# Optimization experiments

Hardware: AMD Instinct MI355X
Metric: run time of the kernel (lower is better)

## Reference

```python
import jax, jax.numpy as jnp
import numpy as np

DIST_THD = 2.0  # squared-distance threshold from my_chamfer_fn


def setup_inputs() -> dict:
    key = jax.random.key(0)
    k1, k2 = jax.random.split(key)
    pc1 = jax.random.normal(k1, (1, 16384, 3), dtype=jnp.float32)
    pc2 = jax.random.normal(k2, (1, 16384, 3), dtype=jnp.float32)
    return {"pc1": pc1, "pc2": pc2}


def _chamfer(x, y):
    # x: (N, P1, D), y: (N, P2, D). Squared pairwise distances (as pytorch3d knn_points).
    x2 = jnp.sum(x * x, axis=-1)                       # (N, P1)
    y2 = jnp.sum(y * y, axis=-1)                       # (N, P2)
    xy = jnp.einsum('npd,nqd->npq', x, y)              # (N, P1, P2)
    d2 = x2[:, :, None] + y2[:, None, :] - 2.0 * xy    # (N, P1, P2)
    cham_x = jnp.min(d2, axis=2)                       # (N, P1) NN dist x->y (K=1)
    cham_y = jnp.min(d2, axis=1)                       # (N, P2) NN dist y->x
    # threshold mask: distances >= 2 are zeroed
    cham_x = jnp.where(cham_x >= DIST_THD, 0.0, cham_x)
    cham_y = jnp.where(cham_y >= DIST_THD, 0.0, cham_y)
    N, P1, _ = x.shape
    P2 = y.shape[1]
    # point_reduction='mean' (lengths are full P), batch_reduction='mean'
    cx = jnp.sum(cham_x, axis=1) / P1
    cy = jnp.sum(cham_y, axis=1) / P2
    return jnp.sum(cx) / N + jnp.sum(cy) / N


def reference(pc1, pc2):
    # Chamfer loss between pc1 and pc2 (the kernel inside NSFP optimization);
    # normals are unused in this code path, so only the distance loss is returned.
    return _chamfer(pc1, pc2)
```

## Files before the change

kernel.cpp:

```cpp
#include <hip/hip_runtime.h>
#include <hip/hip_bf16.h>


constexpr int P      = 16384;
constexpr int BLK    = 256;
constexpr int NSEG   = 8;
constexpr int SEGPTS = P / NSEG;
constexpr int ROUND  = 1024;
constexpr int TILES  = ROUND / 32;
constexpr int ROWSB  = 256;

typedef short s8v  __attribute__((ext_vector_type(8)));
typedef float f16v __attribute__((ext_vector_type(16)));

static __device__ inline unsigned short bf16r(float f) {
    unsigned u = __float_as_uint(f);
    u = (u + 0x7FFFu + ((u >> 16) & 1u)) >> 16;
    return (unsigned short)u;
}
static __device__ inline float bf2f(unsigned short h) {
    return __uint_as_float(((unsigned)h) << 16);
}

static __device__ inline void encA(float a, float b, float c, unsigned e[8]) {
    const unsigned ONE = 0x3F80u;
    const float s = fmaf(a, a, fmaf(b, b, c * c));
    const unsigned short ah = bf16r(a), bh = bf16r(b), ch = bf16r(c);
    const unsigned short al = bf16r(a - bf2f(ah));
    const unsigned short bl = bf16r(b - bf2f(bh));
    const unsigned short cl = bf16r(c - bf2f(ch));
    const unsigned short sh = bf16r(s), sl = bf16r(s - bf2f(sh));
    e[0] = ah | ((unsigned)al << 16);
    e[1] = bh | ((unsigned)bl << 16);
    e[2] = ch | ((unsigned)cl << 16);
    e[3] = ah | ((unsigned)bh << 16);
    e[4] = ch | ((unsigned)sh << 16);
    e[5] = sl | (ONE << 16);
    e[6] = ONE;
    e[7] = 0;
}

static __device__ inline void encB(float a, float b, float c, unsigned e[8]) {
    const unsigned ONE = 0x3F80u;
    const float s = fmaf(a, a, fmaf(b, b, c * c));
    const unsigned short ah = bf16r(a), bh = bf16r(b), ch = bf16r(c);
    const unsigned short al = bf16r(a - bf2f(ah));
    const unsigned short bl = bf16r(b - bf2f(bh));
    const unsigned short cl = bf16r(c - bf2f(ch));
    const unsigned short sh = bf16r(s), sl = bf16r(s - bf2f(sh));
    const unsigned short Ah = bf16r(-2.f * bf2f(ah)), Bh = bf16r(-2.f * bf2f(bh));
    const unsigned short Ch = bf16r(-2.f * bf2f(ch));
    const unsigned short Al = bf16r(-2.f * bf2f(al)), Bl = bf16r(-2.f * bf2f(bl));
    const unsigned short Cl = bf16r(-2.f * bf2f(cl));
    e[0] = Ah | ((unsigned)Ah << 16);
    e[1] = Bh | ((unsigned)Bh << 16);
    e[2] = Ch | ((unsigned)Ch << 16);
    e[3] = Al | ((unsigned)Bl << 16);
    e[4] = Cl | (ONE << 16);
    e[5] = ONE | ((unsigned)sh << 16);
    e[6] = sl;
    e[7] = 0;
}

__global__ __launch_bounds__(BLK, 4) void chamfer_mfma(
    const float* __restrict__ pc1, const float* __restrict__ pc2,
    float* __restrict__ part,
    float* __restrict__ out)
{
    if (blockIdx.x == 0 && blockIdx.y == 0 && blockIdx.z == 0 && threadIdx.x == 0)
        out[0] = 0.0f;

    const int dir = blockIdx.z;
    const float* xs = dir ? pc2 : pc1;
    const float* ys = dir ? pc1 : pc2;

    __shared__ __align__(16) unsigned char ytile[ROUND * 32];

    const int tid  = threadIdx.x;
    const int lane = tid & 63;
    const int wv   = tid >> 6;
    const int l31  = lane & 31;
    const int half = lane >> 5;

    const int rowbase = blockIdx.x * ROWSB + wv * 64;
    s8v afrag[2];
    #pragma unroll
    for (int s = 0; s < 2; ++s) {
        const int p = rowbase + s * 32 + l31;
        unsigned e[8];
        encA(xs[3 * p], xs[3 * p + 1], xs[3 * p + 2], e);
        union { uint4 i; s8v v; } lo, hi;
        lo.i = make_uint4(e[0], e[1], e[2], e[3]);
        hi.i = make_uint4(e[4], e[5], e[6], e[7]);
        afrag[s] = half ? hi.v : lo.v;
    }

    f16v acc0, acc1, Z;
    #pragma unroll
    for (int i = 0; i < 16; ++i) { acc0[i] = 3.0e38f; acc1[i] = 3.0e38f; Z[i] = 0.0f; }

    const int segbase = blockIdx.y * SEGPTS;
    for (int r = 0; r < SEGPTS / ROUND; ++r) {
        #pragma unroll 2
        for (int j = 0; j < ROUND / BLK; ++j) {
            const int i = tid + j * BLK;
            const int q = segbase + r * ROUND + i;
            unsigned e[8];
            encB(ys[3 * q], ys[3 * q + 1], ys[3 * q + 2], e);
            const int tt = i >> 5, cc = i & 31;
            *(uint4*)(ytile + tt * 1024 +       cc * 16) = make_uint4(e[0], e[1], e[2], e[3]);
            *(uint4*)(ytile + tt * 1024 + 512 + cc * 16) = make_uint4(e[4], e[5], e[6], e[7]);
        }
        __syncthreads();

        const unsigned char* rp = ytile + lane * 16;
        #pragma unroll 2
        for (int t = 0; t < TILES; ++t) {
            const s8v bfrag = *(const s8v*)(rp + t * 1024);
            const f16v d0 = __builtin_amdgcn_mfma_f32_32x32x16_bf16(afrag[0], bfrag, Z, 0, 0, 0);
            acc0 = __builtin_elementwise_min(acc0, d0);
            const f16v d1 = __builtin_amdgcn_mfma_f32_32x32x16_bf16(afrag[1], bfrag, Z, 0, 0, 0);
            acc1 = __builtin_elementwise_min(acc1, d1);
        }
        __syncthreads();
    }

    float* pbase = part + ((size_t)(dir * NSEG + blockIdx.y)) * P;
    #pragma unroll
    for (int s = 0; s < 2; ++s) {
        #pragma unroll
        for (int rg = 0; rg < 16; ++rg) {
            float v = s ? acc1[rg] : acc0[rg];
            v = fminf(v, __shfl_xor(v, 1, 64));
            v = fminf(v, __shfl_xor(v, 2, 64));
            v = fminf(v, __shfl_xor(v, 4, 64));
            v = fminf(v, __shfl_xor(v, 8, 64));
            v = fminf(v, __shfl_xor(v, 16, 64));
            if (l31 == 0) {
                const int row = rowbase + s * 32 + (rg & 3) + 8 * (rg >> 2) + 4 * half;
                pbase[row] = v;
            }
        }
    }
}

__global__ __launch_bounds__(BLK) void chamfer_reduce(
    const float* __restrict__ part, float* __restrict__ out)
{
    const int gid = blockIdx.x * BLK + threadIdx.x;
    const int dirbase = (gid >= P) ? NSEG * P : 0;
    const int row = gid & (P - 1);

    float m = part[dirbase + row];
    #pragma unroll
    for (int s = 1; s < NSEG; ++s) m = fminf(m, part[dirbase + s * P + row]);

    if (m >= 2.0f) m = 0.0f;
    float v = m * (1.0f / (float)P);

    #pragma unroll
    for (int off = 32; off > 0; off >>= 1) v += __shfl_down(v, off, 64);

    __shared__ float wsum[BLK / 64];
    const int lane = threadIdx.x & 63;
    const int wvi = threadIdx.x >> 6;
    if (lane == 0) wsum[wvi] = v;
    __syncthreads();
    if (threadIdx.x == 0) {
        float ssum = wsum[0];
        #pragma unroll
        for (int w = 1; w < BLK / 64; ++w) ssum += wsum[w];
        atomicAdd(out, ssum);
    }
}

extern "C" void kernel_launch(void* const* d_in, const int* in_sizes, int n_in,
                              void* d_out, int out_size, void* d_ws, size_t ws_size,
                              hipStream_t stream) {
    const float* pc1 = (const float*)d_in[0];
    const float* pc2 = (const float*)d_in[1];
    float* out = (float*)d_out;
    float* part = (float*)d_ws;

    dim3 grid(P / ROWSB, NSEG, 2);
    chamfer_mfma<<<grid, BLK, 0, stream>>>(pc1, pc2, part, out);
    chamfer_reduce<<<(2 * P) / BLK, BLK, 0, stream>>>(part, out);
}
```

Measured before the change: 83.98 us.

## Precompute bf16 point encodings once in a separate kernel and stream them into LDS

Adds an encode_pts kernel that computes the split-bf16 A and B encodings for both clouds once and writes them to workspace in the tile layout. The main MFMA kernel then loads A fragments directly and copies pre-encoded B tiles into shared memory, instead of re-encoding every y point in each of the 64 row blocks. The inner loop is also unrolled to issue four MFMAs before the min reductions. The cost is an extra kernel launch and about 2 MB of workspace traffic.

```diff
diff --git a/kernel.cpp b/kernel.cpp
--- a/kernel.cpp
+++ b/kernel.cpp
@@ -9,6 +9,7 @@
 constexpr int ROUND  = 1024;
 constexpr int TILES  = ROUND / 32;
 constexpr int ROWSB  = 256;
+constexpr int CLOUDB = P * 32;
 
 typedef short s8v  __attribute__((ext_vector_type(8)));
 typedef float f16v __attribute__((ext_vector_type(16)));
@@ -62,17 +63,40 @@
     e[7] = 0;
 }
 
-__global__ __launch_bounds__(BLK, 4) void chamfer_mfma(
+__global__ __launch_bounds__(BLK) void encode_pts(
     const float* __restrict__ pc1, const float* __restrict__ pc2,
-    float* __restrict__ part,
+    unsigned char* __restrict__ encAbuf, unsigned char* __restrict__ encBbuf,
     float* __restrict__ out)
 {
-    if (blockIdx.x == 0 && blockIdx.y == 0 && blockIdx.z == 0 && threadIdx.x == 0)
-        out[0] = 0.0f;
-
+    const int gid = blockIdx.x * BLK + threadIdx.x;
+    if (gid == 0) out[0] = 0.0f;
+    const int c = gid >> 14;
+    const int p = gid & (P - 1);
+    const float* src = c ? pc2 : pc1;
+    const float x = src[3 * p], y = src[3 * p + 1], z = src[3 * p + 2];
+
+    unsigned ea[8], eb[8];
+    encA(x, y, z, ea);
+    encB(x, y, z, eb);
+
+    unsigned char* ap = encAbuf + (size_t)c * CLOUDB + (size_t)p * 32;
+    *(uint4*)(ap)      = make_uint4(ea[0], ea[1], ea[2], ea[3]);
+    *(uint4*)(ap + 16) = make_uint4(ea[4], ea[5], ea[6], ea[7]);
+
+    unsigned char* bp = encBbuf + (size_t)c * CLOUDB + (size_t)(p >> 5) * 1024
+                        + (size_t)(p & 31) * 16;
+    *(uint4*)(bp)       = make_uint4(eb[0], eb[1], eb[2], eb[3]);
+    *(uint4*)(bp + 512) = make_uint4(eb[4], eb[5], eb[6], eb[7]);
+}
+
+__global__ __launch_bounds__(BLK, 4) void chamfer_mfma(
+    const unsigned char* __restrict__ encAbuf,
+    const unsigned char* __restrict__ encBbuf,
+    float* __restrict__ part)
+{
     const int dir = blockIdx.z;
-    const float* xs = dir ? pc2 : pc1;
-    const float* ys = dir ? pc1 : pc2;
+    const int acloud = dir;
+    const int bcloud = dir ^ 1;
 
     __shared__ __align__(16) unsigned char ytile[ROUND * 32];
 
@@ -83,17 +107,11 @@
     const int half = lane >> 5;
 
     const int rowbase = blockIdx.x * ROWSB + wv * 64;
+    const unsigned char* abase = encAbuf + (size_t)acloud * CLOUDB + (size_t)half * 16;
     s8v afrag[2];
     #pragma unroll
-    for (int s = 0; s < 2; ++s) {
-        const int p = rowbase + s * 32 + l31;
-        unsigned e[8];
-        encA(xs[3 * p], xs[3 * p + 1], xs[3 * p + 2], e);
-        union { uint4 i; s8v v; } lo, hi;
-        lo.i = make_uint4(e[0], e[1], e[2], e[3]);
-        hi.i = make_uint4(e[4], e[5], e[6], e[7]);
-        afrag[s] = half ? hi.v : lo.v;
-    }
+    for (int s = 0; s < 2; ++s)
+        afrag[s] = *(const s8v*)(abase + (size_t)(rowbase + s * 32 + l31) * 32);
 
     f16v acc0, acc1, Z;
     #pragma unroll
@@ -101,26 +119,31 @@
 
     const int segbase = blockIdx.y * SEGPTS;
     for (int r = 0; r < SEGPTS / ROUND; ++r) {
-        #pragma unroll 2
-        for (int j = 0; j < ROUND / BLK; ++j) {
-            const int i = tid + j * BLK;
-            const int q = segbase + r * ROUND + i;
-            unsigned e[8];
-            encB(ys[3 * q], ys[3 * q + 1], ys[3 * q + 2], e);
-            const int tt = i >> 5, cc = i & 31;
-            *(uint4*)(ytile + tt * 1024 +       cc * 16) = make_uint4(e[0], e[1], e[2], e[3]);
-            *(uint4*)(ytile + tt * 1024 + 512 + cc * 16) = make_uint4(e[4], e[5], e[6], e[7]);
+        const uint4* gs = (const uint4*)(encBbuf + (size_t)bcloud * CLOUDB
+                                         + (size_t)(segbase + r * ROUND) * 32);
+        uint4* ls = (uint4*)ytile;
+        #pragma unroll 4
+        for (int j = 0; j < 8; ++j) {
+            const int idx = tid + j * BLK;
+            ls[idx] = gs[idx];
         }
         __syncthreads();
 
         const unsigned char* rp = ytile + lane * 16;
         #pragma unroll 2
-        for (int t = 0; t < TILES; ++t) {
-            const s8v bfrag = *(const s8v*)(rp + t * 1024);
-            const f16v d0 = __builtin_amdgcn_mfma_f32_32x32x16_bf16(afrag[0], bfrag, Z, 0, 0, 0);
-            acc0 = __builtin_elementwise_min(acc0, d0);
-            const f16v d1 = __builtin_amdgcn_mfma_f32_32x32x16_bf16(afrag[1], bfrag, Z, 0, 0, 0);
-            acc1 = __builtin_elementwise_min(acc1, d1);
+        for (int t = 0; t < TILES; t += 2) {
+            const s8v b0 = *(const s8v*)(rp + t * 1024);
+            const s8v b1 = *(const s8v*)(rp + t * 1024 + 1024);
+            const f16v d0a = __builtin_amdgcn_mfma_f32_32x32x16_bf16(afrag[0], b0, Z, 0, 0, 0);
+            const f16v d0b = __builtin_amdgcn_mfma_f32_32x32x16_bf16(afrag[0], b1, Z, 0, 0, 0);
+            #pragma unroll
+            for (int i = 0; i < 16; ++i)
+                acc0[i] = fminf(acc0[i], fminf(d0a[i], d0b[i]));
+            const f16v d1a = __builtin_amdgcn_mfma_f32_32x32x16_bf16(afrag[1], b0, Z, 0, 0, 0);
+            const f16v d1b = __builtin_amdgcn_mfma_f32_32x32x16_bf16(afrag[1], b1, Z, 0, 0, 0);
+            #pragma unroll
+            for (int i = 0; i < 16; ++i)
+                acc1[i] = fminf(acc1[i], fminf(d1a[i], d1b[i]));
         }
         __syncthreads();
     }
@@ -180,9 +203,14 @@
     const float* pc1 = (const float*)d_in[0];
     const float* pc2 = (const float*)d_in[1];
     float* out = (float*)d_out;
-    float* part = (float*)d_ws;
+    unsigned char* ws = (unsigned char*)d_ws;
+    float* part = (float*)ws;
+    unsigned char* encBbuf = ws + (1u << 20);
+    unsigned char* encAbuf = ws + (2u << 20);
+
+    encode_pts<<<(2 * P) / BLK, BLK, 0, stream>>>(pc1, pc2, encAbuf, encBbuf, out);
 
     dim3 grid(P / ROWSB, NSEG, 2);
-    chamfer_mfma<<<grid, BLK, 0, stream>>>(pc1, pc2, part, out);
+    chamfer_mfma<<<grid, BLK, 0, stream>>>(encAbuf, encBbuf, part);
     chamfer_reduce<<<(2 * P) / BLK, BLK, 0, stream>>>(part, out);
 }
```

After: 100.2 us. +19.3%, slower.
